# Kernel tuning notes

Hardware: AMD Instinct MI355X
Metric: run time of the kernel (lower is better)

The kernel has to match this reference:

```python
import jax, jax.numpy as jnp
import numpy as np

B, N, IN_DIM, L = 4, 512, 256, 128


def setup_inputs() -> dict:
    key = jax.random.key(0)
    k1, k2, k3, k4 = jax.random.split(key, 4)
    x = jax.random.normal(k1, (B, N, IN_DIM), dtype=jnp.float32)
    adj = jnp.ones((B, N, N), dtype=jnp.float32)
    box_num = jax.random.randint(k2, (B, 1), 0, N)  # (B,1) int
    # learned params
    W = jax.random.normal(k3, (L, IN_DIM), dtype=jnp.float32) * 0.05  # projection (no bias)
    a = jax.random.uniform(k4, (L,), dtype=jnp.float32)  # adjacency vector, U(0,1)
    return {"x": x, "adj": adj, "box_num": box_num, "W": W, "a": a}


def reference(x, adj, box_num, W, a):
    Bn, Nn, _ = x.shape
    x_hat = jnp.einsum('bnd,ld->bnl', x, W)  # (B,N,L)
    # dynamic mask: -1 where either node is padding, 0 otherwise (B,N,N)
    valid = jnp.arange(Nn)[None, :] < box_num  # (B,N) bool
    pair = valid[:, None, :] & valid[:, :, None]  # (B,N,N)
    mask = jnp.where(pair, 0.0, -1.0).astype(x.dtype)
    # (|x_i - x_j| + mask) . a  ==  |x_i - x_j| . a  +  mask * sum(a)
    diff = jnp.abs(x_hat[:, :, None, :] - x_hat[:, None, :, :])  # (B,N,N,L) big intermediate
    dist = jnp.einsum('bijd,d->bij', diff, a) + mask * jnp.sum(a)
    out = jax.nn.leaky_relu(dist)  # negative_slope 0.01 matches torch default
    out = out - jnp.max(out, axis=-1, keepdims=True)
    soft = adj * jnp.exp(out)
    soft = soft / jnp.sum(soft, axis=-1, keepdims=True) + 1e-10
    return soft
```

## Files before the change

### kernel.cpp

```cpp
#include <hip/hip_runtime.h>
#include <math.h>

namespace {

constexpr int B_ = 4;
constexpr int N_ = 512;
constexpr int D_ = 256;
constexpr int L_ = 128;
constexpr int TI = 4;

__global__ __launch_bounds__(256) void proj_kernel(
    const float* __restrict__ x, const float* __restrict__ W,
    const float* __restrict__ a, float* __restrict__ xs) {
  const int bid = blockIdx.x;
  const int xcd = bid & 7;
  const int b = xcd >> 1;
  const int tile = ((xcd & 1) << 5) + (bid >> 3);
  const int l0 = (tile >> 3) * 16;
  const int n0 = (tile & 7) * 64;

  const int t = threadIdx.x;

  __shared__ float wl_s[16 * 256];
  __shared__ float xl[64 * 129];

  const int n = t & 63;
  const int lg = t >> 6;
  const float* __restrict__ xrow = xl + n * 129;

  {
    const float4* __restrict__ Wsrc =
        reinterpret_cast<const float4*>(W + (size_t)l0 * D_);
    float4* wdst = reinterpret_cast<float4*>(wl_s);
#pragma unroll
    for (int k = 0; k < 4; ++k) wdst[t + k * 256] = Wsrc[t + k * 256];
  }

  float acc[4] = {0.f, 0.f, 0.f, 0.f};

#pragma unroll
  for (int half = 0; half < 2; ++half) {
    __syncthreads();
    {
      const float4* __restrict__ xsrc = reinterpret_cast<const float4*>(
          x + ((size_t)(b * N_ + n0)) * D_ + half * 128);
#pragma unroll
      for (int k = 0; k < 8; ++k) {
        const int idx = t + k * 256;
        const int sn = idx >> 5;
        const int sq = idx & 31;
        const float4 v = xsrc[(size_t)sn * 64 + sq];
        float* dst = xl + sn * 129 + sq * 4;
        dst[0] = v.x; dst[1] = v.y; dst[2] = v.z; dst[3] = v.w;
      }
    }
    __syncthreads();

    const float4* __restrict__ w4 = reinterpret_cast<const float4*>(wl_s);
#pragma unroll 4
    for (int d4 = 0; d4 < 32; ++d4) {
      const float x0 = xrow[d4 * 4 + 0];
      const float x1 = xrow[d4 * 4 + 1];
      const float x2 = xrow[d4 * 4 + 2];
      const float x3 = xrow[d4 * 4 + 3];
#pragma unroll
      for (int k = 0; k < 4; ++k) {
        const float4 w = w4[(lg * 4 + k) * 64 + half * 32 + d4];
        acc[k] += x0 * w.x + x1 * w.y + x2 * w.z + x3 * w.w;
      }
    }
  }

#pragma unroll
  for (int k = 0; k < 4; ++k) {
    const int l = l0 + lg * 4 + k;
    xs[((size_t)(b * L_ + l)) * N_ + n0 + n] = acc[k] * a[l];
  }
}

__global__ __launch_bounds__(512) void dist_softmax_kernel(
    const float* __restrict__ xs, const float* __restrict__ adj,
    const int* __restrict__ box_num, const float* __restrict__ a,
    float* __restrict__ out) {
  const int bid = blockIdx.x;
  const int xcd = bid & 7;
  const int b = xcd >> 1;
  const int tile = ((xcd & 1) << 6) + (bid >> 3);
  const int i0 = tile * TI;

  const int t = threadIdx.x;
  const int j = t;
  const int bn = box_num[b];
  const float* __restrict__ xs_b = xs + (size_t)b * L_ * N_;

  __shared__ float xi_l[L_ * TI];
  __shared__ float red[8][TI];
  __shared__ float sa_l[2];
  __shared__ float rmax_s[TI];
  __shared__ float rsinv_s[TI];

  xi_l[t] = xs_b[(t >> 2) * N_ + i0 + (t & 3)];

  {
    float sa = (t < L_) ? a[t] : 0.f;
#pragma unroll
    for (int off = 1; off < 64; off <<= 1) sa += __shfl_xor(sa, off);
    if (t == 0) sa_l[0] = sa;
    if (t == 64) sa_l[1] = sa;
  }
  __syncthreads();
  const float sum_a = sa_l[0] + sa_l[1];

  float acc[TI];
#pragma unroll
  for (int r = 0; r < TI; ++r) acc[r] = 0.f;

  const float4* __restrict__ xi4 = reinterpret_cast<const float4*>(xi_l);
#pragma unroll
  for (int c = 0; c < 8; ++c) {
    float xj[16];
#pragma unroll
    for (int u = 0; u < 16; ++u) {
      const float* __restrict__ pl = xs_b + (c * 16 + u) * N_;
      xj[u] = pl[j];
    }
#pragma unroll
    for (int u = 0; u < 16; ++u) {
      const float4 xi = xi4[c * 16 + u];
      acc[0] += fabsf(xi.x - xj[u]);
      acc[1] += fabsf(xi.y - xj[u]);
      acc[2] += fabsf(xi.z - xj[u]);
      acc[3] += fabsf(xi.w - xj[u]);
    }
  }

  const bool vj = j < bn;
  float val[TI];
#pragma unroll
  for (int r = 0; r < TI; ++r) {
    const bool vi = (i0 + r) < bn;
    const float d = acc[r] - ((vi && vj) ? 0.f : sum_a);
    val[r] = d >= 0.f ? d : 0.01f * d;
  }

  const int lane = t & 63;
  const int wid = t >> 6;

  {
    float wm[TI];
#pragma unroll
    for (int r = 0; r < TI; ++r) {
      float m = val[r];
#pragma unroll
      for (int off = 1; off < 64; off <<= 1) m = fmaxf(m, __shfl_xor(m, off));
      wm[r] = m;
    }
    if (lane == 0) {
#pragma unroll
      for (int r = 0; r < TI; ++r) red[wid][r] = wm[r];
    }
  }
  __syncthreads();
  if (t < TI) {
    float m = red[0][t];
#pragma unroll
    for (int w = 1; w < 8; ++w) m = fmaxf(m, red[w][t]);
    rmax_s[t] = m;
  }
  __syncthreads();

  float e[TI];
  const float* __restrict__ adjp = adj + ((size_t)(b * N_ + i0)) * N_ + j;
#pragma unroll
  for (int r = 0; r < TI; ++r) {
    e[r] = adjp[(size_t)r * N_] * __expf(val[r] - rmax_s[r]);
  }

  {
    float wsum[TI];
#pragma unroll
    for (int r = 0; r < TI; ++r) {
      float s = e[r];
#pragma unroll
      for (int off = 1; off < 64; off <<= 1) s += __shfl_xor(s, off);
      wsum[r] = s;
    }
    if (lane == 0) {
#pragma unroll
      for (int r = 0; r < TI; ++r) red[wid][r] = wsum[r];
    }
  }
  __syncthreads();
  if (t < TI) {
    float s = red[0][t];
#pragma unroll
    for (int w = 1; w < 8; ++w) s += red[w][t];
    rsinv_s[t] = 1.0f / s;
  }
  __syncthreads();

  float* __restrict__ op = out + ((size_t)(b * N_ + i0)) * N_ + j;
#pragma unroll
  for (int r = 0; r < TI; ++r) {
    op[(size_t)r * N_] = e[r] * rsinv_s[r] + 1e-10f;
  }
}

}

extern "C" void kernel_launch(void* const* d_in, const int* in_sizes, int n_in,
                              void* d_out, int out_size, void* d_ws,
                              size_t ws_size, hipStream_t stream) {
  const float* x = (const float*)d_in[0];
  const float* adj = (const float*)d_in[1];
  const int* box_num = (const int*)d_in[2];
  const float* W = (const float*)d_in[3];
  const float* a = (const float*)d_in[4];
  float* out = (float*)d_out;
  float* xs = (float*)d_ws;

  proj_kernel<<<256, 256, 0, stream>>>(x, W, a, xs);
  dist_softmax_kernel<<<512, 512, 0, stream>>>(xs, adj, box_num, a, out);
}
```

Before: 29.38 us.

## Store scaled projections as packed fp16 and accumulate L1 distances with fdot2

```diff
diff --git a/kernel.cpp b/kernel.cpp
--- a/kernel.cpp
+++ b/kernel.cpp
@@ -1,4 +1,5 @@
 #include <hip/hip_runtime.h>
+#include <hip/hip_fp16.h>
 #include <math.h>
 
 namespace {
@@ -7,11 +8,14 @@
 constexpr int N_ = 512;
 constexpr int D_ = 256;
 constexpr int L_ = 128;
+constexpr int L2_ = L_ / 2;
 constexpr int TI = 4;
+
+typedef _Float16 v2h __attribute__((ext_vector_type(2)));
 
 __global__ __launch_bounds__(256) void proj_kernel(
     const float* __restrict__ x, const float* __restrict__ W,
-    const float* __restrict__ a, float* __restrict__ xs) {
+    const float* __restrict__ a, unsigned* __restrict__ xs_u) {
   const int bid = blockIdx.x;
   const int xcd = bid & 7;
   const int b = xcd >> 1;
@@ -71,15 +75,21 @@
     }
   }
 
-#pragma unroll
-  for (int k = 0; k < 4; ++k) {
-    const int l = l0 + lg * 4 + k;
-    xs[((size_t)(b * L_ + l)) * N_ + n0 + n] = acc[k] * a[l];
-  }
-}
-
-__global__ __launch_bounds__(512) void dist_softmax_kernel(
-    const float* __restrict__ xs, const float* __restrict__ adj,
+  const int lbase = l0 + lg * 4;
+  const float s0 = acc[0] * a[lbase + 0];
+  const float s1 = acc[1] * a[lbase + 1];
+  const float s2 = acc[2] * a[lbase + 2];
+  const float s3 = acc[3] * a[lbase + 3];
+  const auto p01 = __builtin_amdgcn_cvt_pkrtz(s0, s1);
+  const auto p23 = __builtin_amdgcn_cvt_pkrtz(s2, s3);
+  const int l2b = lbase >> 1;
+  unsigned* o = xs_u + ((size_t)b * L2_ + l2b) * N_ + n0 + n;
+  o[0] = __builtin_bit_cast(unsigned, p01);
+  o[(size_t)N_] = __builtin_bit_cast(unsigned, p23);
+}
+
+__global__ __launch_bounds__(512, 4) void dist_softmax_kernel(
+    const unsigned* __restrict__ xs_u, const float* __restrict__ adj,
     const int* __restrict__ box_num, const float* __restrict__ a,
     float* __restrict__ out) {
   const int bid = blockIdx.x;
@@ -91,15 +101,17 @@
   const int t = threadIdx.x;
   const int j = t;
   const int bn = box_num[b];
-  const float* __restrict__ xs_b = xs + (size_t)b * L_ * N_;
-
-  __shared__ float xi_l[L_ * TI];
+  const unsigned* __restrict__ xs_b = xs_u + (size_t)b * L2_ * N_;
+
+  __shared__ unsigned xi_s[L2_ * TI];
   __shared__ float red[8][TI];
   __shared__ float sa_l[2];
   __shared__ float rmax_s[TI];
   __shared__ float rsinv_s[TI];
 
-  xi_l[t] = xs_b[(t >> 2) * N_ + i0 + (t & 3)];
+  if (t < L2_ * TI) {
+    xi_s[t] = xs_b[(t >> 2) * N_ + i0 + (t & 3)];
+  }
 
   {
     float sa = (t < L_) ? a[t] : 0.f;
@@ -115,22 +127,29 @@
 #pragma unroll
   for (int r = 0; r < TI; ++r) acc[r] = 0.f;
 
-  const float4* __restrict__ xi4 = reinterpret_cast<const float4*>(xi_l);
+  const v2h one2 = {(_Float16)1.0f, (_Float16)1.0f};
+  const uint4* __restrict__ xi4 = reinterpret_cast<const uint4*>(xi_s);
+
 #pragma unroll
   for (int c = 0; c < 8; ++c) {
-    float xj[16];
-#pragma unroll
-    for (int u = 0; u < 16; ++u) {
-      const float* __restrict__ pl = xs_b + (c * 16 + u) * N_;
-      xj[u] = pl[j];
-    }
-#pragma unroll
-    for (int u = 0; u < 16; ++u) {
-      const float4 xi = xi4[c * 16 + u];
-      acc[0] += fabsf(xi.x - xj[u]);
-      acc[1] += fabsf(xi.y - xj[u]);
-      acc[2] += fabsf(xi.z - xj[u]);
-      acc[3] += fabsf(xi.w - xj[u]);
+    unsigned xj[8];
+#pragma unroll
+    for (int u = 0; u < 8; ++u) {
+      xj[u] = xs_b[(c * 8 + u) * N_ + j];
+    }
+#pragma unroll
+    for (int u = 0; u < 8; ++u) {
+      const uint4 xi = xi4[c * 8 + u];
+      const unsigned xjw = xj[u];
+      const unsigned xiw[4] = {xi.x, xi.y, xi.z, xi.w};
+#pragma unroll
+      for (int r = 0; r < TI; ++r) {
+        const v2h d = __builtin_bit_cast(v2h, xiw[r]) -
+                      __builtin_bit_cast(v2h, xjw);
+        const unsigned du = __builtin_bit_cast(unsigned, d) & 0x7FFF7FFFu;
+        acc[r] = __builtin_amdgcn_fdot2(__builtin_bit_cast(v2h, du), one2,
+                                        acc[r], false);
+      }
     }
   }
 
@@ -217,8 +236,8 @@
   const float* W = (const float*)d_in[3];
   const float* a = (const float*)d_in[4];
   float* out = (float*)d_out;
-  float* xs = (float*)d_ws;
-
-  proj_kernel<<<256, 256, 0, stream>>>(x, W, a, xs);
-  dist_softmax_kernel<<<512, 512, 0, stream>>>(xs, adj, box_num, a, out);
-}
+  unsigned* xs_u = (unsigned*)d_ws;
+
+  proj_kernel<<<256, 256, 0, stream>>>(x, W, a, xs_u);
+  dist_softmax_kernel<<<512, 512, 0, stream>>>(xs_u, adj, box_num, a, out);
+}
```

New measurement: 24.90 us. -15.2%, faster.
